# Performance work log

Hardware: AMD Instinct MI355X
Metric: run time of the kernel (lower is better)

## Reference

```python
import jax, jax.numpy as jnp
import numpy as np

HIDDEN = 4096
N_HEADS = 32
N_KV = 8
HEAD_DIM = HIDDEN // N_HEADS  # 128
ROT_DIM = int(HEAD_DIM * 0.5)  # partial_rotary_factor = 0.5 -> 64
ROPE_BASE = 1_000_000.0
EPS = 1e-6
T = 2048


def setup_inputs() -> dict:
    key = jax.random.key(0)
    k1, k2, k3, k4, k5 = jax.random.split(key, 5)
    qkv_out = (N_HEADS + 2 * N_KV) * HEAD_DIM  # 6144
    hidden_states = jax.random.normal(k1, (T, HIDDEN), dtype=jnp.float32)
    positions = jnp.arange(T, dtype=jnp.int32)
    w_qkv = jax.random.normal(k2, (HIDDEN, qkv_out), dtype=jnp.float32) * (HIDDEN ** -0.5)
    w_o = jax.random.normal(k3, (N_HEADS * HEAD_DIM, HIDDEN), dtype=jnp.float32) * ((N_HEADS * HEAD_DIM) ** -0.5)
    q_norm_w = jnp.ones((HEAD_DIM,), dtype=jnp.float32) + 0.01 * jax.random.normal(k4, (HEAD_DIM,), dtype=jnp.float32)
    k_norm_w = jnp.ones((HEAD_DIM,), dtype=jnp.float32) + 0.01 * jax.random.normal(k5, (HEAD_DIM,), dtype=jnp.float32)
    return {"hidden_states": hidden_states, "positions": positions,
            "w_qkv": w_qkv, "w_o": w_o, "q_norm_w": q_norm_w, "k_norm_w": k_norm_w}


def _rms_norm(x, w):
    # x: [T, H, D]; normalize over last dim
    var = jnp.mean(jnp.square(x), axis=-1, keepdims=True)
    return x * jax.lax.rsqrt(var + EPS) * w


def _apply_rope(x, positions):
    # neox-style rotary on first ROT_DIM dims of head_dim; rest passes through
    half = ROT_DIM // 2
    inv_freq = 1.0 / (ROPE_BASE ** (jnp.arange(0, ROT_DIM, 2, dtype=jnp.float32) / ROT_DIM))
    freqs = positions.astype(jnp.float32)[:, None] * inv_freq[None, :]  # [T, half]
    cos = jnp.cos(freqs)[:, None, :]  # [T, 1, half]
    sin = jnp.sin(freqs)[:, None, :]
    x_rot, x_pass = x[..., :ROT_DIM], x[..., ROT_DIM:]
    x1, x2 = x_rot[..., :half], x_rot[..., half:]
    rot = jnp.concatenate([x1 * cos - x2 * sin, x2 * cos + x1 * sin], axis=-1)
    return jnp.concatenate([rot, x_pass], axis=-1)


def reference(hidden_states, positions, w_qkv, w_o, q_norm_w, k_norm_w):
    q_size = N_HEADS * HEAD_DIM
    kv_size = N_KV * HEAD_DIM
    qkv = hidden_states @ w_qkv  # [T, q+2kv]
    q = qkv[:, :q_size].reshape(-1, N_HEADS, HEAD_DIM)
    k = qkv[:, q_size:q_size + kv_size].reshape(-1, N_KV, HEAD_DIM)
    v = qkv[:, q_size + kv_size:].reshape(-1, N_KV, HEAD_DIM)
    q = _rms_norm(q, q_norm_w)
    k = _rms_norm(k, k_norm_w)
    q = _apply_rope(q, positions)
    k = _apply_rope(k, positions)
    # GQA: repeat kv heads
    rep = N_HEADS // N_KV
    k = jnp.repeat(k, rep, axis=1)  # [T, H, D]
    v = jnp.repeat(v, rep, axis=1)
    scale = HEAD_DIM ** -0.5
    scores = jnp.einsum('thd,shd->hts', q, k) * scale  # [H, T, T]
    t = hidden_states.shape[0]
    causal = jnp.tril(jnp.ones((t, t), dtype=bool))
    scores = jnp.where(causal[None], scores, jnp.float32(-1e30))
    probs = jax.nn.softmax(scores, axis=-1)
    o = jnp.einsum('hts,shd->thd', probs, v).reshape(t, N_HEADS * HEAD_DIM)
    return o @ w_o
```

## Files before the change

kernel.cpp:

```cpp
#include <hip/hip_runtime.h>
#include <math.h>

#define HIDDEN 4096
#define QKV_N 6144
#define T_LEN 2048
#define HD 128
#define N_HEADS 32
#define N_KV 8
#define SCALE 0.08838834764831845f

typedef unsigned short u16;
typedef unsigned int u32;
typedef __attribute__((ext_vector_type(8))) short bf16x8;
typedef __attribute__((ext_vector_type(4))) float f32x4;

__device__ __forceinline__ u16 f2b(float x) {
  u32 u = __builtin_bit_cast(u32, x);
  u += 0x7fffu + ((u >> 16) & 1u);
  return (u16)(u >> 16);
}

typedef const __attribute__((address_space(1))) void* gas_ptr;
typedef __attribute__((address_space(3))) void* las_ptr;
__device__ __forceinline__ void gll16(const void* g, void* l) {
  __builtin_amdgcn_global_load_lds((gas_ptr)g, (las_ptr)l, 16, 0, 0);
}

__global__ __launch_bounds__(256) void cast_bf16_kernel(
    const float* __restrict__ in, u16* __restrict__ out) {
  const size_t i = ((size_t)blockIdx.x * 256 + threadIdx.x) * 4;
  f32x4 v = *(const f32x4*)(in + i);
  ushort4 o;
  o.x = f2b(v[0]); o.y = f2b(v[1]); o.z = f2b(v[2]); o.w = f2b(v[3]);
  *(ushort4*)(out + i) = o;
}

__global__ __launch_bounds__(256) void transpose_cast_kernel(
    const float* __restrict__ W, u16* __restrict__ WT, int K, int N) {
  __shared__ float t[32][33];
  const int n0 = blockIdx.x * 32, k0 = blockIdx.y * 32;
  const int c = threadIdx.x & 31;
  const int r0 = threadIdx.x >> 5;
#pragma unroll
  for (int j = 0; j < 4; ++j) {
    const int r = r0 + 8 * j;
    t[c][r] = W[(size_t)(k0 + r) * N + n0 + c];
  }
  __syncthreads();
#pragma unroll
  for (int j = 0; j < 4; ++j) {
    const int n = r0 + 8 * j;
    WT[(size_t)(n0 + n) * K + k0 + c] = f2b(t[n][c]);
  }
}

__global__ __launch_bounds__(256) void rope_table_kernel(
    const int* __restrict__ positions, float2* __restrict__ tab) {
  const int i = blockIdx.x * 256 + threadIdx.x;
  const int t = i >> 5, idx = i & 31;
  const float invf = powf(1.0e6f, -(float)idx * (1.0f / 32.0f));
  const float fr = (float)positions[t] * invf;
  tab[i] = make_float2(cosf(fr), sinf(fr));
}

template <int BM, int BN>
__global__ __launch_bounds__(512, 2) void gemm256_kernel(
    const u16* __restrict__ A, const u16* __restrict__ BT,
    float* __restrict__ C, int M, int N, int K) {
  constexpr int WCOLS = BN / 4;
  constexpr int NF = WCOLS / 16;
  constexpr int NF2 = NF / 2;
  constexpr int MF = BM / 32;
  constexpr int ALOADS = BM / 128;
  constexpr int BLOADS = BN / 128;
  constexpr int VMN = ALOADS + BLOADS;
  __shared__ __align__(16) u16 As[2][2][BM * 32];
  __shared__ __align__(16) u16 Bs[2][2][BN * 32];

  const int tid = threadIdx.x;
  const int w = tid >> 6, l = tid & 63;
  const int wr = w >> 2, wc = w & 3;
  const int m = l & 15, g = l >> 4;
  const int bm = blockIdx.y * BM, bn = blockIdx.x * BN;
  const int NT = K >> 6;

  size_t gA[2]; int sA[2];
  size_t gB[2]; int sB[2];
#pragma unroll
  for (int i = 0; i < ALOADS; ++i) {
    const int s = i * 512 + tid;
    const int r = s >> 2, o = s & 3;
    sA[i] = s * 8;
    gA[i] = (size_t)(bm + r) * K + (o ^ ((r >> 1) & 3)) * 8;
  }
#pragma unroll
  for (int i = 0; i < BLOADS; ++i) {
    const int s = i * 512 + tid;
    const int r = s >> 2, o = s & 3;
    sB[i] = s * 8;
    gB[i] = (size_t)(bn + r) * K + (o ^ ((r >> 1) & 3)) * 8;
  }

  const int foff = m * 32 + ((g ^ ((m >> 1) & 3)) * 8);
  const int abase = wr * (BM / 2) * 32;
  const int bbase = wc * WCOLS * 32;

#define STAGE_A(tile, kh)                                                      \
  {                                                                            \
    const size_t kofs = (size_t)(tile) * 64 + (kh) * 32;                       \
    u16* dst = &As[(tile) & 1][kh][0];                                         \
    gll16(A + gA[0] + kofs, dst + sA[0]);                                      \
    if constexpr (ALOADS > 1) gll16(A + gA[1] + kofs, dst + sA[1]);            \
  }
#define STAGE_B(tile, kh)                                                      \
  {                                                                            \
    const size_t kofs = (size_t)(tile) * 64 + (kh) * 32;                       \
    u16* dst = &Bs[(tile) & 1][kh][0];                                         \
    gll16(BT + gB[0] + kofs, dst + sB[0]);                                     \
    if constexpr (BLOADS > 1) gll16(BT + gB[1] + kofs, dst + sB[1]);           \
  }
#define VM_COUNTED()                                                           \
  {                                                                            \
    if constexpr (VMN == 4)                                                    \
      asm volatile("s_waitcnt vmcnt(4)" ::: "memory");                         \
    else                                                                       \
      asm volatile("s_waitcnt vmcnt(3)" ::: "memory");                         \
  }
#define PHASE(j, b, DO_STAGE, tn, VM)                                          \
  {                                                                            \
    constexpr int qn = (j) & 1, kh = (j) >> 1;                                 \
    if constexpr (qn == 0) {                                                   \
      _Pragma("unroll") for (int fm = 0; fm < MF; ++fm)                        \
          af[fm] = *(const bf16x8*)(&As[b][kh][abase + fm * 512 + foff]);      \
    }                                                                          \
    bf16x8 bf[NF2];                                                            \
    _Pragma("unroll") for (int fn = 0; fn < NF2; ++fn)                         \
        bf[fn] =                                                               \
        *(const bf16x8*)(&Bs[b][kh][bbase + (qn * NF2 + fn) * 512 + foff]);    \
    if constexpr (DO_STAGE) {                                                  \
      if constexpr ((j) == 0) STAGE_A(tn, 0);                                  \
      if constexpr ((j) == 1) STAGE_B(tn, 0);                                  \
      if constexpr ((j) == 2) STAGE_A(tn, 1);                                  \
      if constexpr ((j) == 3) STAGE_B(tn, 1);                                  \
    }                                                                          \
    asm volatile("" ::: "memory");                                             \
    __builtin_amdgcn_s_barrier();                                              \
    asm volatile("" ::: "memory");                                             \
    __builtin_amdgcn_s_setprio(1);                                             \
    _Pragma("unroll") for (int fm = 0; fm < MF; ++fm)                          \
        _Pragma("unroll") for (int fn = 0; fn < NF2; ++fn)                     \
        acc[fm][qn * NF2 + fn] = __builtin_amdgcn_mfma_f32_16x16x32_bf16(      \
            af[fm], bf[fn], acc[fm][qn * NF2 + fn], 0, 0, 0);                  \
    __builtin_amdgcn_s_setprio(0);                                             \
    asm volatile("" ::: "memory");                                             \
    if constexpr (((j) & 1) && (VM) == 0)                                      \
      asm volatile("s_waitcnt vmcnt(0)" ::: "memory");                         \
    if constexpr (((j) & 1) && (VM) == 1) VM_COUNTED();                        \
    __builtin_amdgcn_s_barrier();                                              \
    asm volatile("" ::: "memory");                                             \
  }

  f32x4 acc[MF][NF];
#pragma unroll
  for (int i = 0; i < MF; ++i)
#pragma unroll
    for (int j = 0; j < NF; ++j) acc[i][j] = (f32x4){0.f, 0.f, 0.f, 0.f};

  STAGE_A(0, 0); STAGE_B(0, 0); STAGE_A(0, 1); STAGE_B(0, 1);
  VM_COUNTED();
  __builtin_amdgcn_s_barrier();
  asm volatile("" ::: "memory");

  bf16x8 af[MF];
  for (int t = 0; t < NT - 1; ++t) {
    const int b = t & 1, tn = t + 1;
    PHASE(0, b, true, tn, 1);
    PHASE(1, b, true, tn, 1);
    PHASE(2, b, true, tn, 1);
    PHASE(3, b, true, tn, 1);
  }
  {
    const int b = (NT - 1) & 1;
    PHASE(0, b, false, 0, 2);
    PHASE(1, b, false, 0, 0);
    PHASE(2, b, false, 0, 2);
    PHASE(3, b, false, 0, 2);
  }
#undef PHASE
#undef VM_COUNTED
#undef STAGE_B
#undef STAGE_A

#pragma unroll
  for (int fm = 0; fm < MF; ++fm) {
    const int row = bm + wr * (BM / 2) + fm * 16 + g * 4;
#pragma unroll
    for (int fn = 0; fn < NF; ++fn) {
      const int col = bn + wc * WCOLS + fn * 16 + m;
      float* cp = C + (size_t)row * N + col;
#pragma unroll
      for (int r = 0; r < 4; ++r) cp[(size_t)r * N] = acc[fm][fn][r];
    }
  }
}

__global__ __launch_bounds__(128) void normrope_pack_kernel(
    const float* __restrict__ qkv, const float2* __restrict__ tab,
    const float* __restrict__ qw, const float* __restrict__ kw,
    u16* __restrict__ Qp, u16* __restrict__ Kp) {
  const int t = blockIdx.x;
  const int hh = blockIdx.y;
  const int d = threadIdx.x;
  const bool isq = hh < N_HEADS;
  const int col = isq ? hh * HD : HIDDEN + (hh - N_HEADS) * HD;
  const float* row = qkv + (size_t)t * QKV_N + col;
  const float* w = isq ? qw : kw;

  float x = row[d];
  float ss = x * x;
#pragma unroll
  for (int off = 32; off >= 1; off >>= 1) ss += __shfl_xor(ss, off);
  __shared__ float wsum[2];
  __shared__ float xs[128];
  if ((d & 63) == 0) wsum[d >> 6] = ss;
  __syncthreads();
  const float tot = wsum[0] + wsum[1];
  const float inv = rsqrtf(tot * (1.f / 128.f) + 1e-6f);
  const float xn = x * inv * w[d];
  xs[d] = xn;
  __syncthreads();

  float outv;
  if (d < 64) {
    const int idx = d & 31;
    const float2 cs = tab[t * 32 + idx];
    const float x1 = xs[idx], x2 = xs[idx + 32];
    outv = (d < 32) ? (x1 * cs.x - x2 * cs.y) : (x2 * cs.x + x1 * cs.y);
  } else {
    outv = xn;
  }
  if (isq) {
    Qp[((size_t)hh * T_LEN + t) * HD + d] = f2b(outv * SCALE);
  } else {
    Kp[((size_t)(hh - N_HEADS) * T_LEN + t) * HD + d] = f2b(outv);
  }
}

__global__ __launch_bounds__(256) void vtrans_kernel(
    const float* __restrict__ qkv, u16* __restrict__ Vtp) {
  __shared__ float tile[32][132];
  const int t0 = blockIdx.x * 32;
  const int kvh = blockIdx.y;
  const int tv = threadIdx.x >> 3;
  const int c0 = (threadIdx.x & 7) * 16;
  const float* src =
      qkv + (size_t)(t0 + tv) * QKV_N + (HIDDEN + 1024) + kvh * HD + c0;
#pragma unroll
  for (int u = 0; u < 4; ++u)
    *(f32x4*)&tile[tv][c0 + 4 * u] = *(const f32x4*)(src + 4 * u);
  __syncthreads();
  const int dd = threadIdx.x >> 1;
  const int half = threadIdx.x & 1;
  u16 buf[16];
#pragma unroll
  for (int p = 0; p < 16; ++p) buf[p] = f2b(tile[half * 16 + p][dd]);
  u16* dst = Vtp + ((size_t)kvh * HD + dd) * T_LEN + t0 + half * 16;
  *(uint4*)dst = *(uint4*)&buf[0];
  *(uint4*)(dst + 8) = *(uint4*)&buf[8];
}

__global__ __launch_bounds__(256, 3) void attn4_kernel(
    const u16* __restrict__ Qp, const u16* __restrict__ Kp,
    const u16* __restrict__ Vtp, u16* __restrict__ outB) {
  __shared__ __align__(16) u16 Qs[64 * 128];
  __shared__ __align__(16) u16 Ks[2 * 32 * 128];
  __shared__ __align__(16) u16 Vts[2 * 128 * 32];
  __shared__ __align__(16) u16 Plds[4 * 16 * 32];

  const int bx = blockIdx.x;
  const int h = blockIdx.y;
  const int kvh = h >> 2;
  const int tid = threadIdx.x;
  const int w = tid >> 6, l = tid & 63;
  const int g = l >> 4, m = l & 15;

  const u16* kbase = Kp + (size_t)kvh * T_LEN * HD;
  const u16* vbase = Vtp + (size_t)kvh * HD * T_LEN;
  u16* pl = Plds + w * 512;

#define STAGE_KV(jt, b)                                                        \
  {                                                                            \
    _Pragma("unroll") for (int p = 0; p < 2; ++p) {                            \
      const int krow = p * 16 + w * 4 + (l >> 4);                              \
      const int kg = (l & 15) ^ (krow & 7);                                    \
      gll16(kbase + (size_t)((jt) * 32 + krow) * 128 + kg * 8,                 \
            Ks + (b) * 4096 + p * 2048 + w * 512 + l * 8);                     \
      const int dv = p * 64 + w * 16 + (l >> 2);                               \
      const int vg = (l & 3) ^ ((dv >> 1) & 3);                                \
      gll16(vbase + (size_t)dv * T_LEN + (jt) * 32 + vg * 8,                   \
            Vts + (b) * 4096 + p * 2048 + w * 512 + l * 8);                    \
    }                                                                          \
  }

  for (int job = 0; job < 2; ++job) {
    const int qb = job ? bx : 31 - bx;
    const int t0 = qb * 64;
    const int NT = 2 * (qb + 1);

    {
      const u16* qbase = Qp + ((size_t)h * T_LEN + t0) * HD;
#pragma unroll
      for (int p = 0; p < 4; ++p) {
        const int row = p * 16 + w * 4 + (l >> 4);
        const int gr = (l & 15) ^ (row & 7);
        gll16(qbase + row * 128 + gr * 8, Qs + p * 2048 + w * 512 + l * 8);
      }
    }
    STAGE_KV(0, 0);
    __syncthreads();

    bf16x8 qf[4];
    {
      const u16* qr = Qs + (w * 16 + m) * 128;
#pragma unroll
      for (int kk = 0; kk < 4; ++kk)
        qf[kk] = *(const bf16x8*)(qr + (((kk * 4 + g) ^ (m & 7)) * 8));
    }

    f32x4 o[8];
#pragma unroll
    for (int n = 0; n < 8; ++n) o[n] = (f32x4){0.f, 0.f, 0.f, 0.f};
    float mrun = -1e30f, lrun = 0.f;

    for (int jt = 0; jt < NT; ++jt) {
      const int b = jt & 1;
      if (jt + 1 < NT) STAGE_KV(jt + 1, b ^ 1);

      f32x4 s[2];
      s[0] = (f32x4){0.f, 0.f, 0.f, 0.f};
      s[1] = (f32x4){0.f, 0.f, 0.f, 0.f};
      __builtin_amdgcn_s_setprio(1);
#pragma unroll
      for (int f = 0; f < 2; ++f) {
        const u16* kr = Ks + b * 4096 + (f * 16 + m) * 128;
#pragma unroll
        for (int kk = 0; kk < 4; ++kk) {
          bf16x8 kf = *(const bf16x8*)(kr + (((kk * 4 + g) ^ (m & 7)) * 8));
          s[f] =
              __builtin_amdgcn_mfma_f32_16x16x32_bf16(kf, qf[kk], s[f], 0, 0, 0);
        }
      }
      __builtin_amdgcn_s_setprio(0);

      if (jt >= NT - 2) {
        const int qg = t0 + w * 16 + m;
        const int kvb = jt * 32 + g * 4;
#pragma unroll
        for (int f = 0; f < 2; ++f)
#pragma unroll
          for (int r = 0; r < 4; ++r)
            if (kvb + f * 16 + r > qg) s[f][r] = -1e30f;
      }

      float pm = fmaxf(fmaxf(fmaxf(s[0][0], s[0][1]), fmaxf(s[0][2], s[0][3])),
                       fmaxf(fmaxf(s[1][0], s[1][1]), fmaxf(s[1][2], s[1][3])));
      pm = fmaxf(pm, __shfl_xor(pm, 16));
      pm = fmaxf(pm, __shfl_xor(pm, 32));
      if (!__all(pm <= mrun + 8.f)) {
        const float mn = fmaxf(mrun, pm);
        const float sc = __expf(mrun - mn);
        mrun = mn;
        lrun *= sc;
        f32x4 scr;
#pragma unroll
        for (int r = 0; r < 4; ++r) scr[r] = __shfl(sc, g * 4 + r);
#pragma unroll
        for (int n = 0; n < 8; ++n) o[n] *= scr;
      }
      float ps = 0.f;
#pragma unroll
      for (int f = 0; f < 2; ++f)
#pragma unroll
        for (int r = 0; r < 4; ++r) {
          s[f][r] = __expf(s[f][r] - mrun);
          ps += s[f][r];
        }
      ps += __shfl_xor(ps, 16);
      ps += __shfl_xor(ps, 32);
      lrun += ps;

      {
        const u32 a0 = (u32)f2b(s[0][0]) | ((u32)f2b(s[0][1]) << 16);
        const u32 a1 = (u32)f2b(s[0][2]) | ((u32)f2b(s[0][3]) << 16);
        const u32 b0 = (u32)f2b(s[1][0]) | ((u32)f2b(s[1][1]) << 16);
        const u32 b1 = (u32)f2b(s[1][2]) | ((u32)f2b(s[1][3]) << 16);
        *(uint2*)(pl + m * 32 + ((g ^ (m >> 1)) * 4)) = make_uint2(a0, a1);
        *(uint2*)(pl + m * 32 + (((g + 4) ^ (m >> 1)) * 4)) = make_uint2(b0, b1);
      }

      bf16x8 pa;
      {
        const uint2 lo =
            *(const uint2*)(pl + m * 32 + (((2 * g) ^ (m >> 1)) * 4));
        const uint2 hi =
            *(const uint2*)(pl + m * 32 + (((2 * g + 1) ^ (m >> 1)) * 4));
        union { u32 u[4]; bf16x8 v; } pu;
        pu.u[0] = lo.x; pu.u[1] = lo.y; pu.u[2] = hi.x; pu.u[3] = hi.y;
        pa = pu.v;
      }

      __builtin_amdgcn_s_setprio(1);
#pragma unroll
      for (int n = 0; n < 8; ++n) {
        const int dd = n * 16 + m;
        bf16x8 vf = *(const bf16x8*)(Vts + b * 4096 + dd * 32 +
                                     ((g ^ ((dd >> 1) & 3)) * 8));
        o[n] = __builtin_amdgcn_mfma_f32_16x16x32_bf16(pa, vf, o[n], 0, 0, 0);
      }
      __builtin_amdgcn_s_setprio(0);
      __syncthreads();
    }

    float li[4];
#pragma unroll
    for (int r = 0; r < 4; ++r) li[r] = 1.f / __shfl(lrun, g * 4 + r);
    u16* ob = outB + (size_t)(t0 + w * 16 + g * 4) * HIDDEN + h * HD + m;
#pragma unroll
    for (int n = 0; n < 8; ++n)
#pragma unroll
      for (int r = 0; r < 4; ++r)
        ob[(size_t)r * HIDDEN + n * 16] = f2b(o[n][r] * li[r]);
  }
#undef STAGE_KV
}

extern "C" void kernel_launch(void* const* d_in, const int* in_sizes, int n_in,
                              void* d_out, int out_size, void* d_ws,
                              size_t ws_size, hipStream_t stream) {
  const float* hidden = (const float*)d_in[0];
  const int* positions = (const int*)d_in[1];
  const float* w_qkv = (const float*)d_in[2];
  const float* w_o = (const float*)d_in[3];
  const float* q_norm_w = (const float*)d_in[4];
  const float* k_norm_w = (const float*)d_in[5];
  float* out = (float*)d_out;

  u16* hiddenB = (u16*)d_ws;
  u16* Qp = hiddenB;
  u16* wqkvT = hiddenB + (size_t)T_LEN * HIDDEN;
  u16* woT = wqkvT + (size_t)QKV_N * HIDDEN;
  float* qkv = (float*)(woT + (size_t)HIDDEN * HIDDEN);
  u16* attnB = (u16*)(qkv + (size_t)T_LEN * QKV_N);
  u16* Kp = attnB + (size_t)T_LEN * HIDDEN;
  u16* Vtp = Kp + (size_t)N_KV * T_LEN * HD;
  float2* ropeTab = (float2*)(Vtp + (size_t)N_KV * HD * T_LEN);

  cast_bf16_kernel<<<(T_LEN * HIDDEN) / 1024, 256, 0, stream>>>(hidden, hiddenB);
  transpose_cast_kernel<<<dim3(QKV_N / 32, HIDDEN / 32), 256, 0, stream>>>(
      w_qkv, wqkvT, HIDDEN, QKV_N);
  transpose_cast_kernel<<<dim3(HIDDEN / 32, HIDDEN / 32), 256, 0, stream>>>(
      w_o, woT, HIDDEN, HIDDEN);
  rope_table_kernel<<<(T_LEN * 32) / 256, 256, 0, stream>>>(positions, ropeTab);

  gemm256_kernel<256, 256><<<dim3(QKV_N / 256, T_LEN / 256), 512, 0, stream>>>(
      hiddenB, wqkvT, qkv, T_LEN, QKV_N, HIDDEN);
  normrope_pack_kernel<<<dim3(T_LEN, N_HEADS + N_KV), 128, 0, stream>>>(
      qkv, ropeTab, q_norm_w, k_norm_w, Qp, Kp);
  vtrans_kernel<<<dim3(T_LEN / 32, N_KV), 256, 0, stream>>>(qkv, Vtp);
  attn4_kernel<<<dim3(16, N_HEADS), 256, 0, stream>>>(Qp, Kp, Vtp, attnB);
  gemm256_kernel<128, 256><<<dim3(HIDDEN / 256, T_LEN / 128), 512, 0, stream>>>(
      attnB, woT, out, T_LEN, HIDDEN, HIDDEN);
}
```

Baseline: 358.5 us.

## Fold rope table and w_o transpose into QKV GEMM and attention grids

Removes the standalone rope-table and w_o transpose-cast launches. The rope table is now computed by an extra row of blocks added to the QKV GEMM grid. The w_o transpose is done by extra blocks appended to the attention grid, which reuse the Q shared-memory buffer as a transpose tile. This cuts launch overhead and lets the weight transpose overlap with attention, at the cost of extra blocks competing for compute units during those kernels.

```diff
diff --git a/kernel.cpp b/kernel.cpp
--- a/kernel.cpp
+++ b/kernel.cpp
@@ -54,19 +54,23 @@
   }
 }
 
-__global__ __launch_bounds__(256) void rope_table_kernel(
-    const int* __restrict__ positions, float2* __restrict__ tab) {
-  const int i = blockIdx.x * 256 + threadIdx.x;
-  const int t = i >> 5, idx = i & 31;
-  const float invf = powf(1.0e6f, -(float)idx * (1.0f / 32.0f));
-  const float fr = (float)positions[t] * invf;
-  tab[i] = make_float2(cosf(fr), sinf(fr));
-}
-
-template <int BM, int BN>
+template <int BM, int BN, bool ROPE>
 __global__ __launch_bounds__(512, 2) void gemm256_kernel(
     const u16* __restrict__ A, const u16* __restrict__ BT,
-    float* __restrict__ C, int M, int N, int K) {
+    float* __restrict__ C, int M, int N, int K,
+    const int* __restrict__ positions, float2* __restrict__ ropeTab) {
+  if constexpr (ROPE) {
+    if (blockIdx.y == gridDim.y - 1) {
+      for (int i = blockIdx.x * 512 + threadIdx.x; i < T_LEN * 32;
+           i += gridDim.x * 512) {
+        const int t = i >> 5, idx = i & 31;
+        const float invf = powf(1.0e6f, -(float)idx * (1.0f / 32.0f));
+        const float fr = (float)positions[t] * invf;
+        ropeTab[i] = make_float2(cosf(fr), sinf(fr));
+      }
+      return;
+    }
+  }
   constexpr int WCOLS = BN / 4;
   constexpr int NF = WCOLS / 16;
   constexpr int NF2 = NF / 2;
@@ -271,7 +275,8 @@
 
 __global__ __launch_bounds__(256, 3) void attn4_kernel(
     const u16* __restrict__ Qp, const u16* __restrict__ Kp,
-    const u16* __restrict__ Vtp, u16* __restrict__ outB) {
+    const u16* __restrict__ Vtp, u16* __restrict__ outB,
+    const float* __restrict__ w_o, u16* __restrict__ woT) {
   __shared__ __align__(16) u16 Qs[64 * 128];
   __shared__ __align__(16) u16 Ks[2 * 32 * 128];
   __shared__ __align__(16) u16 Vts[2 * 128 * 32];
@@ -279,8 +284,31 @@
 
   const int bx = blockIdx.x;
   const int h = blockIdx.y;
+  const int tid = threadIdx.x;
+
+  if (bx >= 16) {
+    float(*tf)[33] = (float(*)[33])Qs;
+    const int e = (bx - 16) + 8 * h;
+    const int c = tid & 31, rr = tid >> 5;
+    for (int tt = e * 64; tt < e * 64 + 64; ++tt) {
+      const int n0 = (tt & 127) * 32, k0 = (tt >> 7) * 32;
+#pragma unroll
+      for (int j = 0; j < 4; ++j) {
+        const int r = rr + 8 * j;
+        tf[c][r] = w_o[(size_t)(k0 + r) * HIDDEN + n0 + c];
+      }
+      __syncthreads();
+#pragma unroll
+      for (int j = 0; j < 4; ++j) {
+        const int n = rr + 8 * j;
+        woT[(size_t)(n0 + n) * HIDDEN + k0 + c] = f2b(tf[n][c]);
+      }
+      __syncthreads();
+    }
+    return;
+  }
+
   const int kvh = h >> 2;
-  const int tid = threadIdx.x;
   const int w = tid >> 6, l = tid & 63;
   const int g = l >> 4, m = l & 15;
 
@@ -458,16 +486,16 @@
   cast_bf16_kernel<<<(T_LEN * HIDDEN) / 1024, 256, 0, stream>>>(hidden, hiddenB);
   transpose_cast_kernel<<<dim3(QKV_N / 32, HIDDEN / 32), 256, 0, stream>>>(
       w_qkv, wqkvT, HIDDEN, QKV_N);
-  transpose_cast_kernel<<<dim3(HIDDEN / 32, HIDDEN / 32), 256, 0, stream>>>(
-      w_o, woT, HIDDEN, HIDDEN);
-  rope_table_kernel<<<(T_LEN * 32) / 256, 256, 0, stream>>>(positions, ropeTab);
-
-  gemm256_kernel<256, 256><<<dim3(QKV_N / 256, T_LEN / 256), 512, 0, stream>>>(
-      hiddenB, wqkvT, qkv, T_LEN, QKV_N, HIDDEN);
+
+  gemm256_kernel<256, 256, true>
+      <<<dim3(QKV_N / 256, T_LEN / 256 + 1), 512, 0, stream>>>(
+          hiddenB, wqkvT, qkv, T_LEN, QKV_N, HIDDEN, positions, ropeTab);
   normrope_pack_kernel<<<dim3(T_LEN, N_HEADS + N_KV), 128, 0, stream>>>(
       qkv, ropeTab, q_norm_w, k_norm_w, Qp, Kp);
   vtrans_kernel<<<dim3(T_LEN / 32, N_KV), 256, 0, stream>>>(qkv, Vtp);
-  attn4_kernel<<<dim3(16, N_HEADS), 256, 0, stream>>>(Qp, Kp, Vtp, attnB);
-  gemm256_kernel<128, 256><<<dim3(HIDDEN / 256, T_LEN / 128), 512, 0, stream>>>(
-      attnB, woT, out, T_LEN, HIDDEN, HIDDEN);
-}
+  attn4_kernel<<<dim3(24, N_HEADS), 256, 0, stream>>>(Qp, Kp, Vtp, attnB, w_o,
+                                                      woT);
+  gemm256_kernel<128, 256, false>
+      <<<dim3(HIDDEN / 256, T_LEN / 128), 512, 0, stream>>>(
+          attnB, woT, out, T_LEN, HIDDEN, HIDDEN, nullptr, nullptr);
+}
```

Measured after the change: 349.2 us. 1.03x faster.
